# Performance work log

Hardware: AMD Instinct MI355X
Metric: run time of the kernel (lower is better)

Reference implementation:

```python
import jax, jax.numpy as jnp
import numpy as np

B, NQ, NK, D, H = 4, 2048, 2048, 1024, 16
HD = D // H


def setup_inputs() -> dict:
    key = jax.random.key(0)
    ks = jax.random.split(key, 11)
    s = 1.0 / np.sqrt(D)
    return {
        "q": jax.random.normal(ks[0], (B, NQ, D), jnp.float32),
        "k": jax.random.normal(ks[1], (B, NK, D), jnp.float32),
        "v": jax.random.normal(ks[2], (B, NK, D), jnp.float32),
        "Wq": jax.random.uniform(ks[3], (D, D), jnp.float32, -s, s),
        "bq": jax.random.uniform(ks[4], (D,), jnp.float32, -s, s),
        "Wk": jax.random.uniform(ks[5], (D, D), jnp.float32, -s, s),
        "bk": jax.random.uniform(ks[6], (D,), jnp.float32, -s, s),
        "Wv": jax.random.uniform(ks[7], (D, D), jnp.float32, -s, s),
        "bv": jax.random.uniform(ks[8], (D,), jnp.float32, -s, s),
        "Wo": jax.random.uniform(ks[9], (D, D), jnp.float32, -s, s),
        "bo": jax.random.uniform(ks[10], (D,), jnp.float32, -s, s),
    }


def reference(q, k, v, Wq, bq, Wk, bk, Wv, bv, Wo, bo):
    # Linear projections (torch Linear: x @ W.T + b), split into heads [B,H,N,HD]
    qh = (q @ Wq.T + bq).reshape(B, NQ, H, HD).transpose(0, 2, 1, 3)
    kh = (k @ Wk.T + bk).reshape(B, NK, H, HD).transpose(0, 2, 1, 3)
    vh = (v @ Wv.T + bv).reshape(B, NK, H, HD).transpose(0, 2, 1, 3)
    scores = jnp.einsum('bhqd,bhkd->bhqk', qh, kh) / np.sqrt(HD)  # [B,H,Nq,Nk]
    probs = jax.nn.softmax(scores, axis=-1)
    out = jnp.einsum('bhqk,bhkd->bhqd', probs, vh)
    out = out.transpose(0, 2, 1, 3).reshape(B, NQ, D)
    return out @ Wo.T + bo
```

## Files before the change

kernel.cpp:

```cpp
#include <hip/hip_runtime.h>
#include <hip/hip_bf16.h>
#include <cstdint>
#include <cstddef>


typedef __bf16 bf16x8 __attribute__((ext_vector_type(8)));
typedef float f32x4 __attribute__((ext_vector_type(4)));

#define BB 4
#define NQ 2048
#define NK 2048
#define DD 1024
#define HH 16
#define HD 64

#define QSCALE (0.125f * 1.4426950408889634f)

#if __has_builtin(__builtin_amdgcn_exp2f)
#define EXP2F(x) __builtin_amdgcn_exp2f(x)
#else
#define EXP2F(x) exp2f(x)
#endif

__device__ inline void gld_lds16(const void* g, void* lds) {
  __builtin_amdgcn_global_load_lds(
      (__attribute__((address_space(1))) unsigned int*)(g),
      (__attribute__((address_space(3))) unsigned int*)(lds),
      16, 0, 0);
}

__device__ inline bool probe_f32(const void* p) {
  const unsigned short* u = (const unsigned short*)p;
  int bad = 0;
#pragma unroll
  for (int i = 0; i < 64; ++i) {
    const int e = (u[2 * i] >> 7) & 0xFF;
    bad += (e > 0x8F) ? 1 : 0;
  }
  return bad >= 4;
}

__device__ inline bf16x8 cvt8(const float* src) {
  union { bf16x8 v; __hip_bfloat16 h[8]; } u;
#pragma unroll
  for (int j = 0; j < 8; ++j) u.h[j] = __float2bfloat16(src[j]);
  return u.v;
}

__global__ __launch_bounds__(256) void cvt_all(
    const void* __restrict__ q, const void* __restrict__ k,
    const void* __restrict__ v,
    const void* __restrict__ Wq, const void* __restrict__ Wk,
    const void* __restrict__ Wv, const void* __restrict__ Wo,
    __hip_bfloat16* __restrict__ qb, __hip_bfloat16* __restrict__ kb,
    __hip_bfloat16* __restrict__ vb, __hip_bfloat16* __restrict__ Wb) {
  const int bidx = blockIdx.x;
  const void* src; __hip_bfloat16* dst; size_t voff;
  if (bidx < 1536) {
    const int s = bidx >> 9;
    src = s == 0 ? q : (s == 1 ? k : v);
    dst = s == 0 ? qb : (s == 1 ? kb : vb);
    voff = (size_t)(bidx & 511) * 2048;
  } else {
    const int wi = (bidx - 1536) >> 6;
    src = wi == 0 ? Wq : (wi == 1 ? Wk : (wi == 2 ? Wv : Wo));
    dst = Wb + (size_t)wi * (DD * DD);
    voff = (size_t)((bidx - 1536) & 63) * 2048;
  }
  __shared__ int sflag;
  if (threadIdx.x == 0) sflag = probe_f32(src) ? 1 : 0;
  __syncthreads();
  const bool f32 = sflag != 0;
  const int t = threadIdx.x;
#pragma unroll
  for (int i = 0; i < 8; ++i) {
    const size_t j = voff + (size_t)i * 256 + t;
    if (f32) {
      union { f32x4 v2[2]; float f[8]; } u;
      const f32x4* s4 = (const f32x4*)src;
      u.v2[0] = s4[j * 2]; u.v2[1] = s4[j * 2 + 1];
      *(bf16x8*)(dst + j * 8) = cvt8(u.f);
    } else {
      *(f32x4*)(dst + j * 8) = ((const f32x4*)src)[j];
    }
  }
}

__global__ __launch_bounds__(256, 3) void gemm_fast(
    const __hip_bfloat16* __restrict__ qb, const __hip_bfloat16* __restrict__ kb,
    const __hip_bfloat16* __restrict__ vb, const __hip_bfloat16* __restrict__ At,
    const __hip_bfloat16* __restrict__ Wb,
    const void* __restrict__ bq, const void* __restrict__ bk,
    const void* __restrict__ bv, const void* __restrict__ bo,
    const void* __restrict__ WoOrig,
    void* __restrict__ Qp, void* __restrict__ Kp,
    void* __restrict__ Vt, void* __restrict__ Out, int cfg0) {
  __shared__ __align__(16) __hip_bfloat16 sA[128 * 64];
  __shared__ __align__(16) __hip_bfloat16 sB[128 * 64];
  const int t = threadIdx.x;
  const int wave = t >> 6, lane = t & 63;
  const int q4 = lane >> 4, c16 = lane & 15;
  const int xr = c16 & 7;
  const int wr = wave >> 1, wc = wave & 1;

  const int bid = blockIdx.x;
  const int xcd = bid & 7, idx = bid >> 3;
  const int z = idx >> 6;
  const int r6 = idx & 63;
  const int bm = xcd * 8 + (r6 >> 3);
  const int bn = r6 & 7;
  const int cfg = cfg0 + z;

  const __hip_bfloat16* A; const void* biasv; void* Cv; int mode; float scale = 1.f;
  if (cfg == 0)      { A = qb; biasv = bq; Cv = Qp; mode = 0; scale = QSCALE; }
  else if (cfg == 1) { A = kb; biasv = bk; Cv = Kp; mode = 0; }
  else if (cfg == 2) { A = vb; biasv = bv; Cv = Vt; mode = 1; }
  else               { A = At; biasv = bo; Cv = Out; mode = 2; }
  const __hip_bfloat16* Bm = Wb + (size_t)cfg * (DD * DD);

  const bool bias_f32 = probe_f32(biasv);
  const bool c_f32 = (mode == 2) && probe_f32(WoOrig);

  f32x4 acc[4][4];
#pragma unroll
  for (int i = 0; i < 4; ++i)
#pragma unroll
    for (int j = 0; j < 4; ++j) acc[i][j] = (f32x4){0.f, 0.f, 0.f, 0.f};

  const size_t baseA = (size_t)bm * 128 * DD;
  const size_t baseB = (size_t)bn * 128 * DD;

  size_t offA[4], offB[4];
  int lslot[4];
#pragma unroll
  for (int i = 0; i < 4; ++i) {
    const int slot = i * 256 + t;
    const int row = slot >> 3, pg = (slot & 7) ^ (row & 7);
    lslot[i] = slot;
    offA[i] = baseA + (size_t)row * DD + pg * 8;
    offB[i] = baseB + (size_t)row * DD + pg * 8;
  }

  for (int k0 = 0; k0 < DD; k0 += 64) {
    __syncthreads();
#pragma unroll
    for (int i = 0; i < 4; ++i)
      gld_lds16(A + offA[i] + k0, sA + lslot[i] * 8);
#pragma unroll
    for (int i = 0; i < 4; ++i)
      gld_lds16(Bm + offB[i] + k0, sB + lslot[i] * 8);
    __syncthreads();

#pragma unroll
    for (int ks = 0; ks < 2; ++ks) {
      bf16x8 af[4], bfm[4];
#pragma unroll
      for (int rt = 0; rt < 4; ++rt)
        af[rt] = *(const bf16x8*)(sA + (wr * 64 + rt * 16 + c16) * 64 +
                                  ((ks * 4 + q4) ^ xr) * 8);
#pragma unroll
      for (int ct = 0; ct < 4; ++ct)
        bfm[ct] = *(const bf16x8*)(sB + (wc * 64 + ct * 16 + c16) * 64 +
                                   ((ks * 4 + q4) ^ xr) * 8);
#pragma unroll
      for (int rt = 0; rt < 4; ++rt)
#pragma unroll
        for (int ct = 0; ct < 4; ++ct)
          acc[rt][ct] = __builtin_amdgcn_mfma_f32_16x16x32_bf16(af[rt], bfm[ct],
                                                                acc[rt][ct], 0, 0, 0);
    }
  }

  const int row0 = bm * 128 + wr * 64 + q4 * 4;
  const int col0 = bn * 128 + wc * 64 + c16;
#pragma unroll
  for (int ct = 0; ct < 4; ++ct) {
    const int col = col0 + ct * 16;
    const float bvx = bias_f32 ? ((const float*)biasv)[col]
                               : __bfloat162float(((const __hip_bfloat16*)biasv)[col]);
#pragma unroll
    for (int rt = 0; rt < 4; ++rt) {
#pragma unroll
      for (int r = 0; r < 4; ++r) {
        const int row = row0 + rt * 16 + r;
        const float val = (acc[rt][ct][r] + bvx) * scale;
        if (mode == 1) {
          const int b = row >> 11, key = row & 2047;
          const int h = col >> 6, hd = col & 63;
          ((__hip_bfloat16*)Cv)[(size_t)((b * HH + h) * HD + hd) * NK + key] =
              __float2bfloat16(val);
        } else if (c_f32) {
          ((float*)Cv)[(size_t)row * DD + col] = val;
        } else {
          ((__hip_bfloat16*)Cv)[(size_t)row * DD + col] = __float2bfloat16(val);
        }
      }
    }
  }
}

__device__ inline void ld_slot(bool f32, const void* basep, size_t eoff,
                               f32x4& lo, f32x4& hi) {
  if (f32) {
    const f32x4* p = (const f32x4*)((const float*)basep + eoff);
    lo = p[0]; hi = p[1];
  } else {
    lo = *(const f32x4*)((const __hip_bfloat16*)basep + eoff);
  }
}

__device__ inline void st_slot(bool f32, __hip_bfloat16* dst, f32x4 lo, f32x4 hi) {
  if (f32) {
    union { f32x4 v[2]; float f[8]; } u;
    u.v[0] = lo; u.v[1] = hi;
    *(bf16x8*)dst = cvt8(u.f);
  } else {
    *(f32x4*)dst = lo;
  }
}

__global__ __launch_bounds__(256, 3) void gemm_mha(
    const void* __restrict__ qin, const void* __restrict__ kin,
    const void* __restrict__ vin, const void* __restrict__ ain,
    const void* __restrict__ Wq, const void* __restrict__ bq,
    const void* __restrict__ Wk, const void* __restrict__ bk,
    const void* __restrict__ Wv, const void* __restrict__ bv,
    const void* __restrict__ Wo, const void* __restrict__ bo,
    void* __restrict__ Qp, void* __restrict__ Kp,
    void* __restrict__ Vt, void* __restrict__ Out, int cfg0) {
  __shared__ __align__(16) __hip_bfloat16 sA[2][128 * 32];
  __shared__ __align__(16) __hip_bfloat16 sB[2][128 * 32];
  const int t = threadIdx.x;
  const int wave = t >> 6, lane = t & 63;
  const int q4 = lane >> 4, c16 = lane & 15;
  const int wr = wave >> 1, wc = wave & 1;

  const int bid = blockIdx.x;
  const int xcd = bid & 7, idx = bid >> 3;
  const int z = idx >> 6;
  const int r6 = idx & 63;
  const int bm = xcd * 8 + (r6 >> 3);
  const int bn = r6 & 7;
  const int cfg = cfg0 + z;

  const void *Av, *Bv, *biasv; void* Cv; int mode; float scale = 1.f;
  if (cfg == 0)      { Av = qin; Bv = Wq; biasv = bq; Cv = Qp; mode = 0; scale = QSCALE; }
  else if (cfg == 1) { Av = kin; Bv = Wk; biasv = bk; Cv = Kp; mode = 0; }
  else if (cfg == 2) { Av = vin; Bv = Wv; biasv = bv; Cv = Vt; mode = 1; }
  else               { Av = ain; Bv = Wo; biasv = bo; Cv = Out; mode = 2; }

  const bool a_f32 = probe_f32(Av);
  const bool b_f32 = probe_f32(Bv);
  const bool c_f32 = (mode == 2) && b_f32;

  f32x4 acc[4][4];
#pragma unroll
  for (int i = 0; i < 4; ++i)
#pragma unroll
    for (int j = 0; j < 4; ++j) acc[i][j] = (f32x4){0.f, 0.f, 0.f, 0.f};

  const size_t baseA = (size_t)bm * 128 * DD;
  const size_t baseB = (size_t)bn * 128 * DD;
  const int po = ((q4) ^ (c16 & 3)) * 8;

  size_t offA[2], offB[2];
  int lslot[2];
#pragma unroll
  for (int i = 0; i < 2; ++i) {
    const int slot = i * 256 + t;
    const int row = slot >> 2, pg = (slot & 3) ^ (row & 3);
    lslot[i] = slot;
    offA[i] = baseA + (size_t)row * DD + pg * 8;
    offB[i] = baseB + (size_t)row * DD + pg * 8;
  }

  f32x4 Alo[2], Ahi[2], Blo[2], Bhi[2];
#pragma unroll
  for (int i = 0; i < 2; ++i) {
    ld_slot(a_f32, Av, offA[i], Alo[i], Ahi[i]);
    ld_slot(b_f32, Bv, offB[i], Blo[i], Bhi[i]);
  }

  for (int k0 = 0, it = 0; k0 < DD; k0 += 32, ++it) {
    const int p = it & 1;
#pragma unroll
    for (int i = 0; i < 2; ++i) {
      st_slot(a_f32, &sA[p][lslot[i] * 8], Alo[i], Ahi[i]);
      st_slot(b_f32, &sB[p][lslot[i] * 8], Blo[i], Bhi[i]);
    }
    __syncthreads();

    if (k0 + 32 < DD) {
#pragma unroll
      for (int i = 0; i < 2; ++i) {
        ld_slot(a_f32, Av, offA[i] + k0 + 32, Alo[i], Ahi[i]);
        ld_slot(b_f32, Bv, offB[i] + k0 + 32, Blo[i], Bhi[i]);
      }
    }

    bf16x8 af[4], bfm[4];
#pragma unroll
    for (int rt = 0; rt < 4; ++rt)
      af[rt] = *(const bf16x8*)(&sA[p][0] + (wr * 64 + rt * 16 + c16) * 32 + po);
#pragma unroll
    for (int ct = 0; ct < 4; ++ct)
      bfm[ct] = *(const bf16x8*)(&sB[p][0] + (wc * 64 + ct * 16 + c16) * 32 + po);
#pragma unroll
    for (int rt = 0; rt < 4; ++rt)
#pragma unroll
      for (int ct = 0; ct < 4; ++ct)
        acc[rt][ct] = __builtin_amdgcn_mfma_f32_16x16x32_bf16(af[rt], bfm[ct],
                                                              acc[rt][ct], 0, 0, 0);
  }

  const int row0 = bm * 128 + wr * 64 + q4 * 4;
  const int col0 = bn * 128 + wc * 64 + c16;
#pragma unroll
  for (int ct = 0; ct < 4; ++ct) {
    const int col = col0 + ct * 16;
    const float bvx = b_f32 ? ((const float*)biasv)[col]
                            : __bfloat162float(((const __hip_bfloat16*)biasv)[col]);
#pragma unroll
    for (int rt = 0; rt < 4; ++rt) {
#pragma unroll
      for (int r = 0; r < 4; ++r) {
        const int row = row0 + rt * 16 + r;
        const float val = (acc[rt][ct][r] + bvx) * scale;
        if (mode == 1) {
          const int b = row >> 11, key = row & 2047;
          const int h = col >> 6, hd = col & 63;
          ((__hip_bfloat16*)Cv)[(size_t)((b * HH + h) * HD + hd) * NK + key] =
              __float2bfloat16(val);
        } else if (c_f32) {
          ((float*)Cv)[(size_t)row * DD + col] = val;
        } else {
          ((__hip_bfloat16*)Cv)[(size_t)row * DD + col] = __float2bfloat16(val);
        }
      }
    }
  }
}

__global__ __launch_bounds__(256, 3) void flash_attn(
    const __hip_bfloat16* Qp, const __hip_bfloat16* __restrict__ Kp,
    const __hip_bfloat16* __restrict__ Vt, __hip_bfloat16* Ao) {
  __shared__ __align__(16) __hip_bfloat16 sQP[128 * 64];
  __shared__ __align__(16) __hip_bfloat16 sK[2][64 * 64];
  __shared__ __align__(16) __hip_bfloat16 sV[2][64 * 64];

  const int t = threadIdx.x;
  const int wave = t >> 6, lane = t & 63;
  const int q4 = lane >> 4, c16 = lane & 15;
  const int xr = c16 & 7;

  const int bid = blockIdx.x;
  const int xcd = bid & 7, idx = bid >> 3;
  const int bh = xcd * 8 + (idx >> 4);
  const int qt = idx & 15;
  const int b = bh >> 4, h = bh & 15;

#pragma unroll
  for (int i = 0; i < 4; ++i) {
    const int slot = i * 256 + t;
    const int row = slot >> 3, pg = (slot & 7) ^ (row & 7);
    gld_lds16(Qp + ((size_t)(b * NQ + qt * 128 + row) * DD + h * 64 + pg * 8),
              sQP + slot * 8);
  }

  f32x4 o[2][4];
#pragma unroll
  for (int g = 0; g < 2; ++g)
#pragma unroll
    for (int i = 0; i < 4; ++i) o[g][i] = (f32x4){0.f, 0.f, 0.f, 0.f};
  float lp0 = 0.f, lp1 = 0.f;

  __syncthreads();

  bf16x8 aq[2][2];
#pragma unroll
  for (int qg = 0; qg < 2; ++qg)
#pragma unroll
    for (int ks = 0; ks < 2; ++ks)
      aq[qg][ks] = *(const bf16x8*)(sQP + (wave * 32 + qg * 16 + c16) * 64 +
                                    ((ks * 4 + q4) ^ xr) * 8);

#pragma unroll
  for (int i = 0; i < 2; ++i) {
    const int slot = i * 256 + t;
    const int row = slot >> 3, pg = (slot & 7) ^ (row & 7);
    gld_lds16(Kp + ((size_t)(b * NK + row) * DD + h * 64 + pg * 8),
              &sK[0][0] + slot * 8);
    gld_lds16(Vt + ((size_t)(bh * 64 + row) * NK + pg * 8),
              &sV[0][0] + slot * 8);
  }
  __syncthreads();

  const int prow0 = wave * 32 + c16;
  const int prow1 = wave * 32 + 16 + c16;

  for (int kt = 0; kt < NK / 64; ++kt) {
    const int p = kt & 1;
    if (kt + 1 < NK / 64) {
#pragma unroll
      for (int i = 0; i < 2; ++i) {
        const int slot = i * 256 + t;
        const int row = slot >> 3, pg = (slot & 7) ^ (row & 7);
        gld_lds16(Kp + ((size_t)(b * NK + (kt + 1) * 64 + row) * DD + h * 64 + pg * 8),
                  &sK[p ^ 1][0] + slot * 8);
        gld_lds16(Vt + ((size_t)(bh * 64 + row) * NK + (kt + 1) * 64 + pg * 8),
                  &sV[p ^ 1][0] + slot * 8);
      }
    }

    f32x4 s[2][4];
#pragma unroll
    for (int ct = 0; ct < 4; ++ct) {
      bf16x8 bk0 = *(const bf16x8*)(&sK[p][0] + (ct * 16 + c16) * 64 + ((0 + q4) ^ xr) * 8);
      bf16x8 bk1 = *(const bf16x8*)(&sK[p][0] + (ct * 16 + c16) * 64 + ((4 + q4) ^ xr) * 8);
#pragma unroll
      for (int qg = 0; qg < 2; ++qg) {
        f32x4 z = (f32x4){0.f, 0.f, 0.f, 0.f};
        z = __builtin_amdgcn_mfma_f32_16x16x32_bf16(bk0, aq[qg][0], z, 0, 0, 0);
        z = __builtin_amdgcn_mfma_f32_16x16x32_bf16(bk1, aq[qg][1], z, 0, 0, 0);
        s[qg][ct] = z;
      }
    }

#pragma unroll
    for (int qg = 0; qg < 2; ++qg) {
      const int prow = qg ? prow1 : prow0;
#pragma unroll
      for (int ct = 0; ct < 4; ++ct) {
        union { uint2 u; __hip_bfloat16 hx[4]; } pk;
#pragma unroll
        for (int r = 0; r < 4; ++r) {
          const float pe = EXP2F(s[qg][ct][r]);
          if (qg) lp1 += pe; else lp0 += pe;
          pk.hx[r] = __float2bfloat16(pe);
        }
        const int pc = (ct * 2 + (q4 >> 1)) ^ xr;
        *(uint2*)(sQP + prow * 64 + pc * 8 + (q4 & 1) * 4) = pk.u;
      }
    }

#pragma unroll
    for (int kk = 0; kk < 2; ++kk) {
      bf16x8 bvf[4];
#pragma unroll
      for (int ct2 = 0; ct2 < 4; ++ct2)
        bvf[ct2] = *(const bf16x8*)(&sV[p][0] + (ct2 * 16 + c16) * 64 + ((kk * 4 + q4) ^ xr) * 8);
      bf16x8 ap0 = *(const bf16x8*)(sQP + prow0 * 64 + ((kk * 4 + q4) ^ xr) * 8);
      bf16x8 ap1 = *(const bf16x8*)(sQP + prow1 * 64 + ((kk * 4 + q4) ^ xr) * 8);
#pragma unroll
      for (int ct2 = 0; ct2 < 4; ++ct2) {
        o[0][ct2] = __builtin_amdgcn_mfma_f32_16x16x32_bf16(ap0, bvf[ct2], o[0][ct2], 0, 0, 0);
        o[1][ct2] = __builtin_amdgcn_mfma_f32_16x16x32_bf16(ap1, bvf[ct2], o[1][ct2], 0, 0, 0);
      }
    }

    __syncthreads();
  }

  float lr[2][4];
#pragma unroll
  for (int qg = 0; qg < 2; ++qg) {
    float lq = (qg ? lp1 : lp0);
    lq += __shfl_xor(lq, 16, 64);
    lq += __shfl_xor(lq, 32, 64);
    const float linv = 1.f / lq;
#pragma unroll
    for (int r = 0; r < 4; ++r) lr[qg][r] = __shfl(linv, q4 * 4 + r, 64);
  }

#pragma unroll
  for (int qg = 0; qg < 2; ++qg)
#pragma unroll
    for (int ct2 = 0; ct2 < 4; ++ct2)
#pragma unroll
      for (int r = 0; r < 4; ++r) {
        const size_t row = (size_t)(b * NQ + qt * 128 + wave * 32 + qg * 16 + q4 * 4 + r);
        Ao[row * DD + h * 64 + ct2 * 16 + c16] = __float2bfloat16(o[qg][ct2][r] * lr[qg][r]);
      }
}

extern "C" void kernel_launch(void* const* d_in, const int* in_sizes, int n_in,
                              void* d_out, int out_size, void* d_ws, size_t ws_size,
                              hipStream_t stream) {
  const void* q  = d_in[0];
  const void* k  = d_in[1];
  const void* v  = d_in[2];
  const void* Wq = d_in[3];
  const void* bq = d_in[4];
  const void* Wk = d_in[5];
  const void* bk = d_in[6];
  const void* Wv = d_in[7];
  const void* bv = d_in[8];
  const void* Wo = d_in[9];
  const void* bo = d_in[10];

  const size_t MP = (size_t)BB * NQ;
  const size_t MAT = MP * DD;
  __hip_bfloat16* Qp = (__hip_bfloat16*)d_ws;
  __hip_bfloat16* Vt = Qp + MAT;
  __hip_bfloat16* Kp = (__hip_bfloat16*)d_out;
  __hip_bfloat16* At = Qp;

  const size_t NEED = (4 * MAT + 4 * (size_t)(DD * DD)) * sizeof(__hip_bfloat16);
  if (ws_size >= NEED) {
    __hip_bfloat16* kb = Vt + MAT;
    __hip_bfloat16* vb = kb + MAT;
    __hip_bfloat16* Wb = vb + MAT;
    __hip_bfloat16* qb = (__hip_bfloat16*)d_out + MAT;

    cvt_all<<<dim3(1792), 256, 0, stream>>>(q, k, v, Wq, Wk, Wv, Wo,
                                            qb, kb, vb, Wb);
    gemm_fast<<<dim3(1536), 256, 0, stream>>>(qb, kb, vb, At, Wb,
                                              bq, bk, bv, bo, Wo,
                                              Qp, Kp, Vt, d_out, 0);
    flash_attn<<<dim3(1024), 256, 0, stream>>>(Qp, Kp, Vt, At);
    gemm_fast<<<dim3(512), 256, 0, stream>>>(qb, kb, vb, At, Wb,
                                             bq, bk, bv, bo, Wo,
                                             Qp, Kp, Vt, d_out, 3);
  } else {
    gemm_mha<<<dim3(1536), 256, 0, stream>>>(
        q, k, v, At, Wq, bq, Wk, bk, Wv, bv, Wo, bo, Qp, Kp, Vt, d_out, 0);
    flash_attn<<<dim3(1024), 256, 0, stream>>>(Qp, Kp, Vt, At);
    gemm_mha<<<dim3(512), 256, 0, stream>>>(
        q, k, v, At, Wq, bq, Wk, bk, Wv, bv, Wo, bo, Qp, Kp, Vt, d_out, 3);
  }
}
```

Baseline: 386.1 us.

## Stage transposed V projection through LDS and single-buffer V in attention

The GEMM epilogue for the transposed-V projection (mode 1) now writes the tile into swizzled shared memory and emits coalesced 16-byte stores, replacing scattered 2-byte stores. The flash attention kernel drops V double buffering: V is loaded for the current tile at the start of each iteration and an extra barrier is added before the PV step. Raising launch bounds to 4 blocks per CU relies on the smaller LDS footprint for higher occupancy. The risks are exposed V load latency and one more barrier per iteration.

```diff
diff --git a/kernel.cpp b/kernel.cpp
--- a/kernel.cpp
+++ b/kernel.cpp
@@ -171,6 +171,45 @@
     }
   }
 
+  if (mode == 1) {
+    __syncthreads();
+    __hip_bfloat16* sT = wc ? sB : sA;
+#pragma unroll
+    for (int ct = 0; ct < 4; ++ct) {
+      const int col = ct * 16 + c16;
+      const int colg = bn * 128 + wc * 64 + col;
+      const float bvx = bias_f32 ? ((const float*)biasv)[colg]
+                                 : __bfloat162float(((const __hip_bfloat16*)biasv)[colg]);
+      const int sw = (col & 7) << 3;
+#pragma unroll
+      for (int rt = 0; rt < 4; ++rt) {
+        union { uint2 u; __hip_bfloat16 hx[4]; } pk;
+#pragma unroll
+        for (int r = 0; r < 4; ++r)
+          pk.hx[r] = __float2bfloat16((acc[rt][ct][r] + bvx) * scale);
+        const int rowl = wr * 64 + rt * 16 + q4 * 4;
+        *(uint2*)(sT + col * 128 + (rowl ^ sw)) = pk.u;
+      }
+    }
+    __syncthreads();
+    const int bb = bm >> 4;
+    const int kb0 = (bm & 15) * 128;
+#pragma unroll
+    for (int i = 0; i < 8; ++i) {
+      const int idx2 = i * 256 + t;
+      const int half = idx2 >> 10;
+      const int rem = idx2 & 1023;
+      const int col = rem >> 4;
+      const int kc = rem & 15;
+      const __hip_bfloat16* sTh = half ? sB : sA;
+      bf16x8 vv = *(const bf16x8*)(sTh + col * 128 + ((kc * 8) ^ ((col & 7) << 3)));
+      const int hh = bn * 2 + half;
+      *(bf16x8*)((__hip_bfloat16*)Cv +
+                 (size_t)((bb * HH + hh) * HD + col) * NK + kb0 + kc * 8) = vv;
+    }
+    return;
+  }
+
   const int row0 = bm * 128 + wr * 64 + q4 * 4;
   const int col0 = bn * 128 + wc * 64 + c16;
 #pragma unroll
@@ -184,12 +223,7 @@
       for (int r = 0; r < 4; ++r) {
         const int row = row0 + rt * 16 + r;
         const float val = (acc[rt][ct][r] + bvx) * scale;
-        if (mode == 1) {
-          const int b = row >> 11, key = row & 2047;
-          const int h = col >> 6, hd = col & 63;
-          ((__hip_bfloat16*)Cv)[(size_t)((b * HH + h) * HD + hd) * NK + key] =
-              __float2bfloat16(val);
-        } else if (c_f32) {
+        if (c_f32) {
           ((float*)Cv)[(size_t)row * DD + col] = val;
         } else {
           ((__hip_bfloat16*)Cv)[(size_t)row * DD + col] = __float2bfloat16(val);
@@ -341,12 +375,12 @@
   }
 }
 
-__global__ __launch_bounds__(256, 3) void flash_attn(
+__global__ __launch_bounds__(256, 4) void flash_attn(
     const __hip_bfloat16* Qp, const __hip_bfloat16* __restrict__ Kp,
     const __hip_bfloat16* __restrict__ Vt, __hip_bfloat16* Ao) {
   __shared__ __align__(16) __hip_bfloat16 sQP[128 * 64];
   __shared__ __align__(16) __hip_bfloat16 sK[2][64 * 64];
-  __shared__ __align__(16) __hip_bfloat16 sV[2][64 * 64];
+  __shared__ __align__(16) __hip_bfloat16 sV[64 * 64];
 
   const int t = threadIdx.x;
   const int wave = t >> 6, lane = t & 63;
@@ -366,40 +400,43 @@
     gld_lds16(Qp + ((size_t)(b * NQ + qt * 128 + row) * DD + h * 64 + pg * 8),
               sQP + slot * 8);
   }
-
-  f32x4 o[2][4];
-#pragma unroll
-  for (int g = 0; g < 2; ++g)
-#pragma unroll
-    for (int i = 0; i < 4; ++i) o[g][i] = (f32x4){0.f, 0.f, 0.f, 0.f};
-  float lp0 = 0.f, lp1 = 0.f;
-
-  __syncthreads();
-
-  bf16x8 aq[2][2];
-#pragma unroll
-  for (int qg = 0; qg < 2; ++qg)
-#pragma unroll
-    for (int ks = 0; ks < 2; ++ks)
-      aq[qg][ks] = *(const bf16x8*)(sQP + (wave * 32 + qg * 16 + c16) * 64 +
-                                    ((ks * 4 + q4) ^ xr) * 8);
-
 #pragma unroll
   for (int i = 0; i < 2; ++i) {
     const int slot = i * 256 + t;
     const int row = slot >> 3, pg = (slot & 7) ^ (row & 7);
     gld_lds16(Kp + ((size_t)(b * NK + row) * DD + h * 64 + pg * 8),
               &sK[0][0] + slot * 8);
-    gld_lds16(Vt + ((size_t)(bh * 64 + row) * NK + pg * 8),
-              &sV[0][0] + slot * 8);
-  }
+  }
+
+  f32x4 o[2][4];
+#pragma unroll
+  for (int g = 0; g < 2; ++g)
+#pragma unroll
+    for (int i = 0; i < 4; ++i) o[g][i] = (f32x4){0.f, 0.f, 0.f, 0.f};
+  float lp0 = 0.f, lp1 = 0.f;
+
   __syncthreads();
+
+  bf16x8 aq[2][2];
+#pragma unroll
+  for (int qg = 0; qg < 2; ++qg)
+#pragma unroll
+    for (int ks = 0; ks < 2; ++ks)
+      aq[qg][ks] = *(const bf16x8*)(sQP + (wave * 32 + qg * 16 + c16) * 64 +
+                                    ((ks * 4 + q4) ^ xr) * 8);
 
   const int prow0 = wave * 32 + c16;
   const int prow1 = wave * 32 + 16 + c16;
 
   for (int kt = 0; kt < NK / 64; ++kt) {
     const int p = kt & 1;
+#pragma unroll
+    for (int i = 0; i < 2; ++i) {
+      const int slot = i * 256 + t;
+      const int row = slot >> 3, pg = (slot & 7) ^ (row & 7);
+      gld_lds16(Vt + ((size_t)(bh * 64 + row) * NK + kt * 64 + pg * 8),
+                &sV[0] + slot * 8);
+    }
     if (kt + 1 < NK / 64) {
 #pragma unroll
       for (int i = 0; i < 2; ++i) {
@@ -407,8 +444,6 @@
         const int row = slot >> 3, pg = (slot & 7) ^ (row & 7);
         gld_lds16(Kp + ((size_t)(b * NK + (kt + 1) * 64 + row) * DD + h * 64 + pg * 8),
                   &sK[p ^ 1][0] + slot * 8);
-        gld_lds16(Vt + ((size_t)(bh * 64 + row) * NK + (kt + 1) * 64 + pg * 8),
-                  &sV[p ^ 1][0] + slot * 8);
       }
     }
 
@@ -443,12 +478,14 @@
       }
     }
 
+    __syncthreads();
+
 #pragma unroll
     for (int kk = 0; kk < 2; ++kk) {
       bf16x8 bvf[4];
 #pragma unroll
       for (int ct2 = 0; ct2 < 4; ++ct2)
-        bvf[ct2] = *(const bf16x8*)(&sV[p][0] + (ct2 * 16 + c16) * 64 + ((kk * 4 + q4) ^ xr) * 8);
+        bvf[ct2] = *(const bf16x8*)(&sV[0] + (ct2 * 16 + c16) * 64 + ((kk * 4 + q4) ^ xr) * 8);
       bf16x8 ap0 = *(const bf16x8*)(sQP + prow0 * 64 + ((kk * 4 + q4) ^ xr) * 8);
       bf16x8 ap1 = *(const bf16x8*)(sQP + prow1 * 64 + ((kk * 4 + q4) ^ xr) * 8);
 #pragma unroll
```

After: 338.9 us. -12.2%, faster.
